# Kernel optimization log

Hardware: AMD Instinct MI355X
Metric: run time of the kernel (lower is better)

The kernel has to match this reference:

```python
import jax, jax.numpy as jnp
import numpy as np

TAU_MIN, TAU_MAX, TAU_SMALL, N_REF = 0.005, 0.1, 0.3, 4


def _l2norm(x, eps=1e-12):
    # matches torch F.normalize: x / max(||x||_2, eps)
    n = jnp.linalg.norm(x, axis=-1, keepdims=True)
    return x / jnp.maximum(n, eps)


def setup_inputs() -> dict:
    key = jax.random.key(0)
    k1, k2, k3 = jax.random.split(key, 3)
    B, C, H, W = 8, 384, 40, 40
    feats = jax.random.normal(k1, (B, C, H, W), dtype=jnp.float32)
    refs = jax.random.normal(k2, (N_REF, B, C, H, W), dtype=jnp.float32)
    sopm = jax.random.uniform(k3, (B, 1, 160, 160), dtype=jnp.float32)
    log_tau = jnp.array([np.log(0.03)], dtype=jnp.float32)
    alpha_raw = jnp.array([0.0], dtype=jnp.float32)
    return {"feats": feats, "refs": refs, "sopm": sopm,
            "log_tau": log_tau, "alpha_raw": alpha_raw}


def reference(feats, refs, sopm, log_tau, alpha_raw):
    B, C, H, W = feats.shape
    N = H * W
    # buffer contents and SOPM cache are detached in the torch module
    refs = jax.lax.stop_gradient(refs)
    sopm = jax.lax.stop_gradient(sopm)

    tau = jnp.clip(jnp.exp(log_tau[0]), TAU_MIN, TAU_MAX)
    alpha = jax.nn.sigmoid(alpha_raw[0])

    tokens = feats.reshape(B, C, N).transpose(0, 2, 1)   # [B, N, C]
    cur_n = _l2norm(tokens)

    n_ref = refs.shape[0]
    warped_sum = jnp.zeros_like(tokens)
    for r in range(n_ref):  # fixed small ref-frame loop (n_ref=4)
        ref_tok = refs[r].reshape(B, C, N).transpose(0, 2, 1)  # [B, N, C]
        ref_n = _l2norm(ref_tok)
        sim = jnp.einsum('bnc,bmc->bnm', cur_n, ref_n)          # cosine sims
        w = jax.nn.softmax(sim / tau, axis=-1)                  # [B, N, N]
        warped_sum = warped_sum + jnp.einsum('bnm,bmc->bnc', w, ref_tok)
    warped = warped_sum / n_ref

    # SOPM(t-1) -> bilinear resize (align_corners=False) -> threshold mask
    sopm_r = jax.image.resize(sopm, (B, 1, H, W), method='bilinear')
    mask = (sopm_r.reshape(B, 1, N).transpose(0, 2, 1) > TAU_SMALL).astype(feats.dtype)  # [B,N,1]

    alpha_eff = alpha  # full buffer: n_avail == n_ref
    fused = alpha_eff * warped + (1.0 - alpha_eff) * tokens
    enhanced = mask * fused + (1.0 - mask) * tokens
    return enhanced.transpose(0, 2, 1).reshape(B, C, H, W)
```

## Files before the change

### kernel.cpp

```cpp
#include <hip/hip_runtime.h>
#include <stdint.h>

#define B_  8
#define C_  384
#define N_  1600
#define R_  4
#define S_  160
#define HW_ 40

typedef float  f32x4  __attribute__((ext_vector_type(4)));
typedef __bf16 bf16x8 __attribute__((ext_vector_type(8)));
typedef long long i64t;

__device__ __forceinline__ unsigned short f2bf(float x){
  __bf16 h = (__bf16)x;
  return __builtin_bit_cast(unsigned short, h);
}
__device__ __forceinline__ float bf2f(unsigned short u){
  return __builtin_bit_cast(float, (uint32_t)u << 16);
}
__device__ __forceinline__ uint32_t pk_fp8x4(float a, float b, float c, float d){
  int lo = __builtin_amdgcn_cvt_pk_fp8_f32(a, b, 0, false);
  int hi = __builtin_amdgcn_cvt_pk_fp8_f32(c, d, 0, false);
  return (uint32_t)(lo & 0xffff) | ((uint32_t)hi << 16);
}

__device__ __forceinline__ void gload_lds16(const void* g, void* l){
  __builtin_amdgcn_global_load_lds(
      (const __attribute__((address_space(1))) uint32_t*)g,
      (__attribute__((address_space(3))) uint32_t*)l, 16, 0, 0);
}

__global__ void prep_kernel(const float* __restrict__ feats,
                            const float* __restrict__ refs,
                            unsigned char* __restrict__ Qb,
                            unsigned char* __restrict__ Kb,
                            unsigned short* __restrict__ Vb){
  int nt = blockIdx.x, mat = blockIdx.y;
  __shared__ unsigned short tile[64][386];
  __shared__ float ssp[64][17];
  __shared__ float inv_sh[64];
  int t = threadIdx.x;
  bool isref = (mat >= B_);
  const float* src = isref ? refs  + (size_t)(mat - B_) * C_ * N_
                           : feats + (size_t)mat * C_ * N_;
  int n4  = t & 15;
  int crb = t >> 4;
  float ss4[4] = {0.f, 0.f, 0.f, 0.f};
#pragma unroll
  for (int ct = 0; ct < 6; ++ct){
#pragma unroll
    for (int i = 0; i < 4; ++i){
      int c = ct * 64 + crb + 16 * i;
      size_t off = (size_t)c * N_ + nt * 64 + n4 * 4;
      float4 v = *(const float4*)(src + off);
      ushort4 o;
      o.x = f2bf(v.x); o.y = f2bf(v.y); o.z = f2bf(v.z); o.w = f2bf(v.w);
      if (isref){
        unsigned short* vdst = Vb + (size_t)(mat - B_) * C_ * N_;
        *(ushort4*)(vdst + off) = o;
      }
      tile[n4*4+0][c] = o.x;
      tile[n4*4+1][c] = o.y;
      tile[n4*4+2][c] = o.z;
      tile[n4*4+3][c] = o.w;
      ss4[0] += v.x * v.x;  ss4[1] += v.y * v.y;
      ss4[2] += v.z * v.z;  ss4[3] += v.w * v.w;
    }
  }
#pragma unroll
  for (int j = 0; j < 4; ++j) ssp[n4*4+j][crb] = ss4[j];
  __syncthreads();
  if (t < 64){
    float s = 0.f;
#pragma unroll
    for (int p = 0; p < 16; ++p) s += ssp[t][p];
    inv_sh[t] = 1.f / fmaxf(sqrtf(s), 1e-12f);
  }
  __syncthreads();
  unsigned char* dst = isref ? Kb + (size_t)(mat - B_) * N_ * C_
                             : Qb + (size_t)mat * N_ * C_;
#pragma unroll
  for (int i = 0; i < 4; ++i){
    int nr = (t >> 4) + 16 * i;
    float iv = inv_sh[nr];
    unsigned char* drow = dst + (size_t)(nt * 64 + nr) * C_;
#pragma unroll
    for (int ct = 0; ct < 6; ++ct){
      int c0 = ct * 64 + (t & 15) * 4;
      uint32_t a0 = *(const uint32_t*)(&tile[nr][c0]);
      uint32_t a1 = *(const uint32_t*)(&tile[nr][c0 + 2]);
      uint32_t pk = pk_fp8x4(bf2f((unsigned short)(a0 & 0xffff)) * iv,
                             bf2f((unsigned short)(a0 >> 16))    * iv,
                             bf2f((unsigned short)(a1 & 0xffff)) * iv,
                             bf2f((unsigned short)(a1 >> 16))    * iv);
      *(uint32_t*)(drow + c0) = pk;
    }
  }
}

__global__ void mask_kernel(const float* __restrict__ sopm,
                            float* __restrict__ maskp){
  int gid = blockIdx.x * 256 + threadIdx.x;
  int b = gid / N_, n = gid - b * N_;
  int oy = n / HW_, ox = n - oy * HW_;
  const float* sp = sopm + (size_t)b * S_ * S_;
  float cy = oy * 4 + 1.5f, cx = ox * 4 + 1.5f;
  int y0 = 4*oy - 2; if (y0 < 0) y0 = 0;
  int y1 = 4*oy + 5; if (y1 > S_-1) y1 = S_-1;
  int x0 = 4*ox - 2; if (x0 < 0) x0 = 0;
  int x1 = 4*ox + 5; if (x1 > S_-1) x1 = S_-1;
  float wsy = 0.f, wsx = 0.f;
  for (int j = y0; j <= y1; ++j) wsy += 1.f - fabsf(j - cy) * 0.25f;
  for (int j = x0; j <= x1; ++j) wsx += 1.f - fabsf(j - cx) * 0.25f;
  float acc = 0.f;
  for (int jy = y0; jy <= y1; ++jy){
    float wy = 1.f - fabsf(jy - cy) * 0.25f;
    float rs = 0.f;
    for (int jx = x0; jx <= x1; ++jx)
      rs += (1.f - fabsf(jx - cx) * 0.25f) * sp[jy * S_ + jx];
    acc += wy * rs;
  }
  float val = acc / (wsy * wsx);
  maskp[gid] = (val > 0.3f) ? 1.f : 0.f;
}

#define KB0_   0
#define KB1_   12288
#define VB_    24576
#define P_OFF  49152
#define LDS_SZ 53248

__global__ __launch_bounds__(256, 2) void attn_kernel(
    const unsigned char* __restrict__ Qb,
    const unsigned char* __restrict__ Kb,
    const unsigned short* __restrict__ Vb,
    const float* __restrict__ log_tau,
    unsigned short* __restrict__ Or)
{
  __shared__ __align__(16) char lds[LDS_SZ];
  int wg   = blockIdx.x;
  int orig = (wg & 7) * 100 + (wg >> 3);
  int qt   = orig % 25;
  int rb   = orig / 25;
  int b    = rb & 7;
  int tid  = threadIdx.x;
  int lane = tid & 63;
  int w    = tid >> 6;
  int mw   = w >> 1;
  int qw   = w & 1;
  int l15  = lane & 15;
  int lg   = lane >> 4;

  float tau = expf(log_tau[0]);
  tau = fminf(fmaxf(tau, 0.005f), 0.1f);
  float sc = 1.4426950408889634f / tau;

  i64t qreg[2][12];
#pragma unroll
  for (int qt2 = 0; qt2 < 2; ++qt2){
    const unsigned char* qp = Qb +
        ((size_t)b * N_ + qt * 64 + qw * 32 + qt2 * 16 + l15) * C_ + lg * 8;
#pragma unroll
    for (int ks = 0; ks < 12; ++ks)
      qreg[qt2][ks] = *(const i64t*)(qp + ks * 32);
  }

  f32x4 o[4][6];
#pragma unroll
  for (int i = 0; i < 4; ++i)
#pragma unroll
    for (int j = 0; j < 6; ++j) o[i][j] = (f32x4){0.f,0.f,0.f,0.f};
  float lsum0 = 0.f, lsum1 = 0.f;

  const unsigned char*  kmat = Kb + (size_t)rb * N_ * C_;
  const unsigned short* vmat = Vb + (size_t)rb * C_ * N_;
  char* Pb = lds + P_OFF;

  int koffB[3];
#pragma unroll
  for (int i = 0; i < 3; ++i){
    int L = (w * 3 + i) * 64 + lane;
    int m   = L / 24;
    int pos = L - m * 24;
    int cc  = (pos >> 3) * 8 + ((pos & 7) ^ (m & 7));
    koffB[i] = m * C_ + cc * 16;
  }
  int voff[6];
#pragma unroll
  for (int i = 0; i < 6; ++i){
    int chunk = (w * 6 + i) * 64 + lane;
    int line = chunk >> 3;
    int u    = (chunk & 7) ^ (line & 7);
    voff[i]  = (line * 2 + (u >> 2)) * N_ + (u & 3) * 8;
  }

  const int s_l  = (l15 >> 1) & 3;
  const int p_w0 = (qw*32      + l15) * 64 + (((2*mw + (lg >> 1)) ^ s_l) << 4) + (lg & 1) * 8;
  const int p_w1 = (qw*32 + 16 + l15) * 64 + (((2*mw + (lg >> 1)) ^ s_l) << 4) + (lg & 1) * 8;
  const int p_rc = ((lg ^ s_l) << 4) + l15 * 64;

  auto stageK = [&](int t, int buf){
    const unsigned char* kb = kmat + (size_t)t * 32 * C_;
    char* kdst = lds + (buf ? KB1_ : KB0_) + w * 3072;
#pragma unroll
    for (int i = 0; i < 3; ++i) gload_lds16(kb + koffB[i], kdst + i * 1024);
  };
  auto stageV = [&](int t){
    const unsigned short* vb = vmat + t * 32;
    char* vdst = lds + VB_ + w * 6144;
#pragma unroll
    for (int i = 0; i < 6; ++i) gload_lds16(vb + voff[i], vdst + i * 1024);
  };

  stageK(0, 0);
  stageV(0);
  stageK(1, 1);
  asm volatile("s_waitcnt vmcnt(9)" ::: "memory");
  __builtin_amdgcn_sched_barrier(0);
  __builtin_amdgcn_s_barrier();
  __builtin_amdgcn_sched_barrier(0);

  const int krow = (mw * 16 + l15);
  for (int mt = 0; mt < 50; ++mt){
    int cur = mt & 1;
    const char* kbR = lds + (cur ? KB1_ : KB0_);

    f32x4 s0 = {0.f,0.f,0.f,0.f}, s1 = {0.f,0.f,0.f,0.f};
    __builtin_amdgcn_s_setprio(1);
#pragma unroll
    for (int ks = 0; ks < 12; ++ks){
      int lc  = 2 * ks + (lg >> 1);
      int off = ((lc >> 3) * 8 + ((lc & 7) ^ (krow & 7))) * 16 + (lg & 1) * 8;
      i64t a = *(const i64t*)(kbR + krow * 384 + off);
      s0 = __builtin_amdgcn_mfma_f32_16x16x32_fp8_fp8(a, qreg[0][ks], s0, 0, 0, 0);
      s1 = __builtin_amdgcn_mfma_f32_16x16x32_fp8_fp8(a, qreg[1][ks], s1, 0, 0, 0);
    }
    __builtin_amdgcn_s_setprio(0);

    ushort4 pw0, pw1;
    {
      __bf16 h;
      float l0 = 0.f, l1 = 0.f;
      h = (__bf16)exp2f((s0[0]-1.f)*sc); l0 += (float)h; pw0.x = __builtin_bit_cast(unsigned short, h);
      h = (__bf16)exp2f((s0[1]-1.f)*sc); l0 += (float)h; pw0.y = __builtin_bit_cast(unsigned short, h);
      h = (__bf16)exp2f((s0[2]-1.f)*sc); l0 += (float)h; pw0.z = __builtin_bit_cast(unsigned short, h);
      h = (__bf16)exp2f((s0[3]-1.f)*sc); l0 += (float)h; pw0.w = __builtin_bit_cast(unsigned short, h);
      h = (__bf16)exp2f((s1[0]-1.f)*sc); l1 += (float)h; pw1.x = __builtin_bit_cast(unsigned short, h);
      h = (__bf16)exp2f((s1[1]-1.f)*sc); l1 += (float)h; pw1.y = __builtin_bit_cast(unsigned short, h);
      h = (__bf16)exp2f((s1[2]-1.f)*sc); l1 += (float)h; pw1.z = __builtin_bit_cast(unsigned short, h);
      h = (__bf16)exp2f((s1[3]-1.f)*sc); l1 += (float)h; pw1.w = __builtin_bit_cast(unsigned short, h);
      lsum0 += l0; lsum1 += l1;
    }
    *(ushort4*)(Pb + p_w0) = pw0;
    *(ushort4*)(Pb + p_w1) = pw1;
    asm volatile("s_waitcnt lgkmcnt(0) vmcnt(0)" ::: "memory");
    __builtin_amdgcn_sched_barrier(0);
    __builtin_amdgcn_s_barrier();
    __builtin_amdgcn_sched_barrier(0);

    int tk = (mt + 2 < 50) ? mt + 2 : mt;
    stageK(tk, cur);
    __builtin_amdgcn_sched_barrier(0);

    bf16x8 pa[4];
#pragma unroll
    for (int qf2 = 0; qf2 < 4; ++qf2)
      pa[qf2] = *(const bf16x8*)(Pb + qf2 * 1024 + p_rc);
    __builtin_amdgcn_s_setprio(1);
#pragma unroll
    for (int cf = 0; cf < 6; ++cf){
      int c  = w * 96 + cf * 16 + l15;
      int vo = (c >> 1) * 128 + (((lg | ((c & 1) << 2)) ^ ((c >> 1) & 7)) << 4);
      bf16x8 vf = *(const bf16x8*)(lds + VB_ + vo);
#pragma unroll
      for (int qf2 = 0; qf2 < 4; ++qf2)
        o[qf2][cf] = __builtin_amdgcn_mfma_f32_16x16x32_bf16(pa[qf2], vf, o[qf2][cf], 0, 0, 0);
    }
    __builtin_amdgcn_s_setprio(0);

    __builtin_amdgcn_sched_barrier(0);
    __builtin_amdgcn_s_barrier();
    __builtin_amdgcn_sched_barrier(0);

    int tv = (mt + 1 < 50) ? mt + 1 : 49;
    stageV(tv);
    __builtin_amdgcn_sched_barrier(0);
  }

  lsum0 += __shfl_xor(lsum0, 16, 64);
  lsum0 += __shfl_xor(lsum0, 32, 64);
  lsum1 += __shfl_xor(lsum1, 16, 64);
  lsum1 += __shfl_xor(lsum1, 32, 64);
  __syncthreads();
  float* lsh = (float*)lds;
  if (lg == 0){
    lsh[mw * 64 + qw * 32 + l15]      = lsum0;
    lsh[mw * 64 + qw * 32 + 16 + l15] = lsum1;
  }
  __syncthreads();
  float invl[4][4];
#pragma unroll
  for (int qf2 = 0; qf2 < 4; ++qf2)
#pragma unroll
    for (int rg = 0; rg < 4; ++rg){
      int q = qf2 * 16 + lg * 4 + rg;
      invl[qf2][rg] = 1.f / (lsh[q] + lsh[64 + q]);
    }

  int qbase = qt * 64;
  unsigned short* op = Or + ((size_t)rb * N_ + qbase) * C_ + w * 96 + l15;
#pragma unroll
  for (int qf2 = 0; qf2 < 4; ++qf2){
#pragma unroll
    for (int cf = 0; cf < 6; ++cf){
#pragma unroll
      for (int rg = 0; rg < 4; ++rg){
        int q = qf2 * 16 + lg * 4 + rg;
        op[(size_t)q * C_ + cf * 16] = f2bf(o[qf2][cf][rg] * invl[qf2][rg]);
      }
    }
  }
}

__global__ void combine_kernel(const unsigned short* __restrict__ Or,
                               const float* __restrict__ feats,
                               const float* __restrict__ maskp,
                               const float* __restrict__ alpha_raw,
                               float* __restrict__ out){
  int nt = blockIdx.x, ct = blockIdx.y, b = blockIdx.z;
  __shared__ float tile[64][65];
  float alpha = 1.f / (1.f + expf(-alpha_raw[0]));
  int t = threadIdx.x;
#pragma unroll
  for (int i = 0; i < 4; ++i){
    int chunk = t + 256 * i;
    int nr = chunk >> 4, c4 = chunk & 15;
    size_t base = ((size_t)b * N_ + nt * 64 + nr) * C_ + ct * 64 + c4 * 4;
    float4 s = {0.f,0.f,0.f,0.f};
#pragma unroll
    for (int r = 0; r < 4; ++r){
      ushort4 v = *(const ushort4*)(Or + (size_t)r * B_ * N_ * C_ + base);
      s.x += bf2f(v.x); s.y += bf2f(v.y); s.z += bf2f(v.z); s.w += bf2f(v.w);
    }
    tile[nr][c4*4+0] = s.x; tile[nr][c4*4+1] = s.y;
    tile[nr][c4*4+2] = s.z; tile[nr][c4*4+3] = s.w;
  }
  __syncthreads();
#pragma unroll
  for (int i = 0; i < 4; ++i){
    int chunk = t + 256 * i;
    int cr = chunk >> 4, n4 = chunk & 15;
    size_t fb = ((size_t)b * C_ + ct * 64 + cr) * N_ + nt * 64 + n4 * 4;
    float4 f  = *(const float4*)(feats + fb);
    float4 mk = *(const float4*)(maskp + (size_t)b * N_ + nt * 64 + n4 * 4);
    float4 ov;
    ov.x = f.x + mk.x * alpha * (tile[n4*4+0][cr] * 0.25f - f.x);
    ov.y = f.y + mk.y * alpha * (tile[n4*4+1][cr] * 0.25f - f.y);
    ov.z = f.z + mk.z * alpha * (tile[n4*4+2][cr] * 0.25f - f.z);
    ov.w = f.w + mk.w * alpha * (tile[n4*4+3][cr] * 0.25f - f.w);
    *(float4*)(out + fb) = ov;
  }
}

__global__ void poison_kernel(float* out, int n){
  int i = blockIdx.x * 256 + threadIdx.x;
  if (i < n) out[i] = 1.0e6f;
}

extern "C" void kernel_launch(void* const* d_in, const int* in_sizes, int n_in,
                              void* d_out, int out_size, void* d_ws, size_t ws_size,
                              hipStream_t stream){
  const float* feats     = (const float*)d_in[0];
  const float* refs      = (const float*)d_in[1];
  const float* sopm      = (const float*)d_in[2];
  const float* log_tau   = (const float*)d_in[3];
  const float* alpha_raw = (const float*)d_in[4];
  float* out = (float*)d_out;

  const size_t SZ_MASK = (size_t)B_ * N_ * 4;
  const size_t SZ_QB   = (size_t)B_ * N_ * C_;
  const size_t SZ_KB   = (size_t)R_ * B_ * N_ * C_;
  const size_t SZ_VB   = (size_t)R_ * B_ * N_ * C_ * 2;
  const size_t SZ_OR   = (size_t)R_ * B_ * N_ * C_ * 2;
  const size_t need = SZ_MASK + SZ_QB + SZ_KB + SZ_VB + SZ_OR;

  if (ws_size < need){
    poison_kernel<<<(out_size + 255) / 256, 256, 0, stream>>>(out, out_size);
    return;
  }
  char* ws = (char*)d_ws;
  float*          maskp = (float*)ws;
  unsigned char*  Qb    = (unsigned char*)(ws + SZ_MASK);
  unsigned char*  Kb    = (unsigned char*)(ws + SZ_MASK + SZ_QB);
  unsigned short* Vb    = (unsigned short*)(ws + SZ_MASK + SZ_QB + SZ_KB);
  unsigned short* Or    = (unsigned short*)(ws + SZ_MASK + SZ_QB + SZ_KB + SZ_VB);

  mask_kernel   <<<50, 256, 0, stream>>>(sopm, maskp);
  prep_kernel   <<<dim3(25, 40), 256, 0, stream>>>(feats, refs, Qb, Kb, Vb);
  attn_kernel   <<<800, 256, 0, stream>>>(Qb, Kb, Vb, log_tau, Or);
  combine_kernel<<<dim3(25, 6, 8), 256, 0, stream>>>(Or, feats, maskp, alpha_raw, out);
}
```

Before: 202.3 us.

## Split attention work across 8 waves per block with smaller per-wave tiles

Moves the attention kernel from 256 to 512 threads per block. Each wave now owns 16 queries instead of 32 for the QK step and 48 channels instead of 96 for the PV step, which halves the per-wave accumulator and Q registers. The goal is more resident waves per CU to hide latency. In exchange, K staging is limited to four waves and the prologue prefetch becomes a full wait, which reduces overlap, while the per-block barriers now synchronise more waves.

```diff
diff --git a/kernel.cpp b/kernel.cpp
--- a/kernel.cpp
+++ b/kernel.cpp
@@ -131,7 +131,7 @@
 #define P_OFF  49152
 #define LDS_SZ 53248
 
-__global__ __launch_bounds__(256, 2) void attn_kernel(
+__global__ __launch_bounds__(512, 4) void attn_kernel(
     const unsigned char* __restrict__ Qb,
     const unsigned char* __restrict__ Kb,
     const unsigned short* __restrict__ Vb,
@@ -147,8 +147,8 @@
   int tid  = threadIdx.x;
   int lane = tid & 63;
   int w    = tid >> 6;
-  int mw   = w >> 1;
-  int qw   = w & 1;
+  int mw   = w >> 2;
+  int qw   = w & 3;
   int l15  = lane & 15;
   int lg   = lane >> 4;
 
@@ -156,22 +156,21 @@
   tau = fminf(fmaxf(tau, 0.005f), 0.1f);
   float sc = 1.4426950408889634f / tau;
 
-  i64t qreg[2][12];
-#pragma unroll
-  for (int qt2 = 0; qt2 < 2; ++qt2){
+  i64t qreg[12];
+  {
     const unsigned char* qp = Qb +
-        ((size_t)b * N_ + qt * 64 + qw * 32 + qt2 * 16 + l15) * C_ + lg * 8;
+        ((size_t)b * N_ + qt * 64 + qw * 16 + l15) * C_ + lg * 8;
 #pragma unroll
     for (int ks = 0; ks < 12; ++ks)
-      qreg[qt2][ks] = *(const i64t*)(qp + ks * 32);
-  }
-
-  f32x4 o[4][6];
+      qreg[ks] = *(const i64t*)(qp + ks * 32);
+  }
+
+  f32x4 o[4][3];
 #pragma unroll
   for (int i = 0; i < 4; ++i)
 #pragma unroll
-    for (int j = 0; j < 6; ++j) o[i][j] = (f32x4){0.f,0.f,0.f,0.f};
-  float lsum0 = 0.f, lsum1 = 0.f;
+    for (int j = 0; j < 3; ++j) o[i][j] = (f32x4){0.f,0.f,0.f,0.f};
+  float lsum = 0.f;
 
   const unsigned char*  kmat = Kb + (size_t)rb * N_ * C_;
   const unsigned short* vmat = Vb + (size_t)rb * C_ * N_;
@@ -180,80 +179,75 @@
   int koffB[3];
 #pragma unroll
   for (int i = 0; i < 3; ++i){
-    int L = (w * 3 + i) * 64 + lane;
+    int L = ((w & 3) * 3 + i) * 64 + lane;
     int m   = L / 24;
     int pos = L - m * 24;
     int cc  = (pos >> 3) * 8 + ((pos & 7) ^ (m & 7));
     koffB[i] = m * C_ + cc * 16;
   }
-  int voff[6];
-#pragma unroll
-  for (int i = 0; i < 6; ++i){
-    int chunk = (w * 6 + i) * 64 + lane;
+  int voff[3];
+#pragma unroll
+  for (int i = 0; i < 3; ++i){
+    int chunk = (w * 3 + i) * 64 + lane;
     int line = chunk >> 3;
     int u    = (chunk & 7) ^ (line & 7);
     voff[i]  = (line * 2 + (u >> 2)) * N_ + (u & 3) * 8;
   }
 
   const int s_l  = (l15 >> 1) & 3;
-  const int p_w0 = (qw*32      + l15) * 64 + (((2*mw + (lg >> 1)) ^ s_l) << 4) + (lg & 1) * 8;
-  const int p_w1 = (qw*32 + 16 + l15) * 64 + (((2*mw + (lg >> 1)) ^ s_l) << 4) + (lg & 1) * 8;
+  const int p_w  = (qw*16 + l15) * 64 + (((mw*2 + (lg >> 1)) ^ s_l) << 4) + (lg & 1) * 8;
   const int p_rc = ((lg ^ s_l) << 4) + l15 * 64;
 
   auto stageK = [&](int t, int buf){
-    const unsigned char* kb = kmat + (size_t)t * 32 * C_;
-    char* kdst = lds + (buf ? KB1_ : KB0_) + w * 3072;
-#pragma unroll
-    for (int i = 0; i < 3; ++i) gload_lds16(kb + koffB[i], kdst + i * 1024);
+    if (w < 4){
+      const unsigned char* kb = kmat + (size_t)t * 32 * C_;
+      char* kdst = lds + (buf ? KB1_ : KB0_) + w * 3072;
+#pragma unroll
+      for (int i = 0; i < 3; ++i) gload_lds16(kb + koffB[i], kdst + i * 1024);
+    }
   };
   auto stageV = [&](int t){
     const unsigned short* vb = vmat + t * 32;
-    char* vdst = lds + VB_ + w * 6144;
-#pragma unroll
-    for (int i = 0; i < 6; ++i) gload_lds16(vb + voff[i], vdst + i * 1024);
+    char* vdst = lds + VB_ + w * 3072;
+#pragma unroll
+    for (int i = 0; i < 3; ++i) gload_lds16(vb + voff[i], vdst + i * 1024);
   };
 
   stageK(0, 0);
   stageV(0);
-  stageK(1, 1);
-  asm volatile("s_waitcnt vmcnt(9)" ::: "memory");
+  asm volatile("s_waitcnt vmcnt(0)" ::: "memory");
   __builtin_amdgcn_sched_barrier(0);
   __builtin_amdgcn_s_barrier();
   __builtin_amdgcn_sched_barrier(0);
+  stageK(1, 1);
 
   const int krow = (mw * 16 + l15);
   for (int mt = 0; mt < 50; ++mt){
     int cur = mt & 1;
     const char* kbR = lds + (cur ? KB1_ : KB0_);
 
-    f32x4 s0 = {0.f,0.f,0.f,0.f}, s1 = {0.f,0.f,0.f,0.f};
+    f32x4 s0 = {0.f,0.f,0.f,0.f};
     __builtin_amdgcn_s_setprio(1);
 #pragma unroll
     for (int ks = 0; ks < 12; ++ks){
       int lc  = 2 * ks + (lg >> 1);
       int off = ((lc >> 3) * 8 + ((lc & 7) ^ (krow & 7))) * 16 + (lg & 1) * 8;
       i64t a = *(const i64t*)(kbR + krow * 384 + off);
-      s0 = __builtin_amdgcn_mfma_f32_16x16x32_fp8_fp8(a, qreg[0][ks], s0, 0, 0, 0);
-      s1 = __builtin_amdgcn_mfma_f32_16x16x32_fp8_fp8(a, qreg[1][ks], s1, 0, 0, 0);
+      s0 = __builtin_amdgcn_mfma_f32_16x16x32_fp8_fp8(a, qreg[ks], s0, 0, 0, 0);
     }
     __builtin_amdgcn_s_setprio(0);
 
-    ushort4 pw0, pw1;
+    ushort4 pw;
     {
       __bf16 h;
-      float l0 = 0.f, l1 = 0.f;
-      h = (__bf16)exp2f((s0[0]-1.f)*sc); l0 += (float)h; pw0.x = __builtin_bit_cast(unsigned short, h);
-      h = (__bf16)exp2f((s0[1]-1.f)*sc); l0 += (float)h; pw0.y = __builtin_bit_cast(unsigned short, h);
-      h = (__bf16)exp2f((s0[2]-1.f)*sc); l0 += (float)h; pw0.z = __builtin_bit_cast(unsigned short, h);
-      h = (__bf16)exp2f((s0[3]-1.f)*sc); l0 += (float)h; pw0.w = __builtin_bit_cast(unsigned short, h);
-      h = (__bf16)exp2f((s1[0]-1.f)*sc); l1 += (float)h; pw1.x = __builtin_bit_cast(unsigned short, h);
-      h = (__bf16)exp2f((s1[1]-1.f)*sc); l1 += (float)h; pw1.y = __builtin_bit_cast(unsigned short, h);
-      h = (__bf16)exp2f((s1[2]-1.f)*sc); l1 += (float)h; pw1.z = __builtin_bit_cast(unsigned short, h);
-      h = (__bf16)exp2f((s1[3]-1.f)*sc); l1 += (float)h; pw1.w = __builtin_bit_cast(unsigned short, h);
-      lsum0 += l0; lsum1 += l1;
-    }
-    *(ushort4*)(Pb + p_w0) = pw0;
-    *(ushort4*)(Pb + p_w1) = pw1;
+      float l0 = 0.f;
+      h = (__bf16)exp2f((s0[0]-1.f)*sc); l0 += (float)h; pw.x = __builtin_bit_cast(unsigned short, h);
+      h = (__bf16)exp2f((s0[1]-1.f)*sc); l0 += (float)h; pw.y = __builtin_bit_cast(unsigned short, h);
+      h = (__bf16)exp2f((s0[2]-1.f)*sc); l0 += (float)h; pw.z = __builtin_bit_cast(unsigned short, h);
+      h = (__bf16)exp2f((s0[3]-1.f)*sc); l0 += (float)h; pw.w = __builtin_bit_cast(unsigned short, h);
+      lsum += l0;
+    }
+    *(ushort4*)(Pb + p_w) = pw;
     asm volatile("s_waitcnt lgkmcnt(0) vmcnt(0)" ::: "memory");
     __builtin_amdgcn_sched_barrier(0);
     __builtin_amdgcn_s_barrier();
@@ -269,8 +263,8 @@
       pa[qf2] = *(const bf16x8*)(Pb + qf2 * 1024 + p_rc);
     __builtin_amdgcn_s_setprio(1);
 #pragma unroll
-    for (int cf = 0; cf < 6; ++cf){
-      int c  = w * 96 + cf * 16 + l15;
+    for (int cf = 0; cf < 3; ++cf){
+      int c  = w * 48 + cf * 16 + l15;
       int vo = (c >> 1) * 128 + (((lg | ((c & 1) << 2)) ^ ((c >> 1) & 7)) << 4);
       bf16x8 vf = *(const bf16x8*)(lds + VB_ + vo);
 #pragma unroll
@@ -288,16 +282,11 @@
     __builtin_amdgcn_sched_barrier(0);
   }
 
-  lsum0 += __shfl_xor(lsum0, 16, 64);
-  lsum0 += __shfl_xor(lsum0, 32, 64);
-  lsum1 += __shfl_xor(lsum1, 16, 64);
-  lsum1 += __shfl_xor(lsum1, 32, 64);
+  lsum += __shfl_xor(lsum, 16, 64);
+  lsum += __shfl_xor(lsum, 32, 64);
   __syncthreads();
   float* lsh = (float*)lds;
-  if (lg == 0){
-    lsh[mw * 64 + qw * 32 + l15]      = lsum0;
-    lsh[mw * 64 + qw * 32 + 16 + l15] = lsum1;
-  }
+  if (lg == 0) lsh[mw * 64 + qw * 16 + l15] = lsum;
   __syncthreads();
   float invl[4][4];
 #pragma unroll
@@ -309,11 +298,11 @@
     }
 
   int qbase = qt * 64;
-  unsigned short* op = Or + ((size_t)rb * N_ + qbase) * C_ + w * 96 + l15;
+  unsigned short* op = Or + ((size_t)rb * N_ + qbase) * C_ + w * 48 + l15;
 #pragma unroll
   for (int qf2 = 0; qf2 < 4; ++qf2){
 #pragma unroll
-    for (int cf = 0; cf < 6; ++cf){
+    for (int cf = 0; cf < 3; ++cf){
 #pragma unroll
       for (int rg = 0; rg < 4; ++rg){
         int q = qf2 * 16 + lg * 4 + rg;
@@ -398,6 +387,6 @@
 
   mask_kernel   <<<50, 256, 0, stream>>>(sopm, maskp);
   prep_kernel   <<<dim3(25, 40), 256, 0, stream>>>(feats, refs, Qb, Kb, Vb);
-  attn_kernel   <<<800, 256, 0, stream>>>(Qb, Kb, Vb, log_tau, Or);
+  attn_kernel   <<<800, 512, 0, stream>>>(Qb, Kb, Vb, log_tau, Or);
   combine_kernel<<<dim3(25, 6, 8), 256, 0, stream>>>(Or, feats, maskp, alpha_raw, out);
 }
```

Measured after the change: 217.6 us. +7.5%, slower.

## Double the KV tile to 64 keys per iteration and single-buffer K

Applied to the files above, without the earlier changes.

The attention loop now handles 64 key positions per iteration instead of 32, cutting the iteration count and barrier count in half. Each wave computes two 16-row key fragments for the QK product and two k-slices for the PV product. K goes from double buffering to a single larger buffer, and V and P layouts are reswizzled for the 64-wide tiles. This raises LDS use to 80KB, which may limit occupancy at two blocks per CU, and it adds a barrier after the V stage, which reduces overlap between loads and compute.

```diff
diff --git a/kernel.cpp b/kernel.cpp
--- a/kernel.cpp
+++ b/kernel.cpp
@@ -125,11 +125,10 @@
   maskp[gid] = (val > 0.3f) ? 1.f : 0.f;
 }
 
-#define KB0_   0
-#define KB1_   12288
+#define KB_    0
 #define VB_    24576
-#define P_OFF  49152
-#define LDS_SZ 53248
+#define P_OFF  73728
+#define LDS_SZ 81920
 
 __global__ __launch_bounds__(256, 2) void attn_kernel(
     const unsigned char* __restrict__ Qb,
@@ -151,6 +150,7 @@
   int qw   = w & 1;
   int l15  = lane & 15;
   int lg   = lane >> 4;
+  const int s7 = l15 & 7;
 
   float tau = expf(log_tau[0]);
   tau = fminf(fmaxf(tau, 0.005f), 0.1f);
@@ -177,105 +177,124 @@
   const unsigned short* vmat = Vb + (size_t)rb * C_ * N_;
   char* Pb = lds + P_OFF;
 
-  int koffB[3];
-#pragma unroll
-  for (int i = 0; i < 3; ++i){
-    int L = (w * 3 + i) * 64 + lane;
+  int koffB[6];
+#pragma unroll
+  for (int i = 0; i < 6; ++i){
+    int L = (w * 6 + i) * 64 + lane;
     int m   = L / 24;
     int pos = L - m * 24;
     int cc  = (pos >> 3) * 8 + ((pos & 7) ^ (m & 7));
     koffB[i] = m * C_ + cc * 16;
   }
-  int voff[6];
-#pragma unroll
-  for (int i = 0; i < 6; ++i){
-    int chunk = (w * 6 + i) * 64 + lane;
-    int line = chunk >> 3;
-    int u    = (chunk & 7) ^ (line & 7);
-    voff[i]  = (line * 2 + (u >> 2)) * N_ + (u & 3) * 8;
-  }
-
-  const int s_l  = (l15 >> 1) & 3;
-  const int p_w0 = (qw*32      + l15) * 64 + (((2*mw + (lg >> 1)) ^ s_l) << 4) + (lg & 1) * 8;
-  const int p_w1 = (qw*32 + 16 + l15) * 64 + (((2*mw + (lg >> 1)) ^ s_l) << 4) + (lg & 1) * 8;
-  const int p_rc = ((lg ^ s_l) << 4) + l15 * 64;
-
-  auto stageK = [&](int t, int buf){
-    const unsigned char* kb = kmat + (size_t)t * 32 * C_;
-    char* kdst = lds + (buf ? KB1_ : KB0_) + w * 3072;
-#pragma unroll
-    for (int i = 0; i < 3; ++i) gload_lds16(kb + koffB[i], kdst + i * 1024);
+  int voff[12];
+#pragma unroll
+  for (int i = 0; i < 12; ++i){
+    int chunk = (w * 12 + i) * 64 + lane;
+    int c = chunk >> 3;
+    int u = (chunk & 7) ^ (c & 7);
+    voff[i] = c * N_ + u * 8;
+  }
+
+  int p_wo[2][2];
+#pragma unroll
+  for (int mi = 0; mi < 2; ++mi)
+#pragma unroll
+    for (int qi = 0; qi < 2; ++qi)
+      p_wo[mi][qi] = (qw*32 + qi*16 + l15) * 128 +
+                     (((mw*4 + mi*2 + (lg >> 1)) ^ s7) << 4) + (lg & 1) * 8;
+
+  auto stageK = [&](int t){
+    const unsigned char* kb = kmat + (size_t)t * 64 * C_;
+#pragma unroll
+    for (int i = 0; i < 6; ++i)
+      gload_lds16(kb + koffB[i], lds + KB_ + (w * 6 + i) * 1024);
   };
   auto stageV = [&](int t){
-    const unsigned short* vb = vmat + t * 32;
-    char* vdst = lds + VB_ + w * 6144;
-#pragma unroll
-    for (int i = 0; i < 6; ++i) gload_lds16(vb + voff[i], vdst + i * 1024);
+    const unsigned short* vb = vmat + t * 64;
+#pragma unroll
+    for (int i = 0; i < 12; ++i)
+      gload_lds16(vb + voff[i], lds + VB_ + (w * 12 + i) * 1024);
   };
 
-  stageK(0, 0);
+  stageK(0);
   stageV(0);
-  stageK(1, 1);
-  asm volatile("s_waitcnt vmcnt(9)" ::: "memory");
+  asm volatile("s_waitcnt vmcnt(0)" ::: "memory");
   __builtin_amdgcn_sched_barrier(0);
   __builtin_amdgcn_s_barrier();
   __builtin_amdgcn_sched_barrier(0);
 
-  const int krow = (mw * 16 + l15);
-  for (int mt = 0; mt < 50; ++mt){
-    int cur = mt & 1;
-    const char* kbR = lds + (cur ? KB1_ : KB0_);
-
-    f32x4 s0 = {0.f,0.f,0.f,0.f}, s1 = {0.f,0.f,0.f,0.f};
+  const int krow0 = (mw * 32 + l15) * 384;
+  const int krow1 = (mw * 32 + 16 + l15) * 384;
+  for (int mt = 0; mt < 25; ++mt){
+    f32x4 s00 = {0.f,0.f,0.f,0.f}, s01 = {0.f,0.f,0.f,0.f};
+    f32x4 s10 = {0.f,0.f,0.f,0.f}, s11 = {0.f,0.f,0.f,0.f};
     __builtin_amdgcn_s_setprio(1);
 #pragma unroll
     for (int ks = 0; ks < 12; ++ks){
       int lc  = 2 * ks + (lg >> 1);
-      int off = ((lc >> 3) * 8 + ((lc & 7) ^ (krow & 7))) * 16 + (lg & 1) * 8;
-      i64t a = *(const i64t*)(kbR + krow * 384 + off);
-      s0 = __builtin_amdgcn_mfma_f32_16x16x32_fp8_fp8(a, qreg[0][ks], s0, 0, 0, 0);
-      s1 = __builtin_amdgcn_mfma_f32_16x16x32_fp8_fp8(a, qreg[1][ks], s1, 0, 0, 0);
+      int off = ((lc >> 3) * 8 + ((lc & 7) ^ s7)) * 16 + (lg & 1) * 8;
+      i64t a0 = *(const i64t*)(lds + KB_ + krow0 + off);
+      i64t a1 = *(const i64t*)(lds + KB_ + krow1 + off);
+      s00 = __builtin_amdgcn_mfma_f32_16x16x32_fp8_fp8(a0, qreg[0][ks], s00, 0, 0, 0);
+      s01 = __builtin_amdgcn_mfma_f32_16x16x32_fp8_fp8(a0, qreg[1][ks], s01, 0, 0, 0);
+      s10 = __builtin_amdgcn_mfma_f32_16x16x32_fp8_fp8(a1, qreg[0][ks], s10, 0, 0, 0);
+      s11 = __builtin_amdgcn_mfma_f32_16x16x32_fp8_fp8(a1, qreg[1][ks], s11, 0, 0, 0);
     }
     __builtin_amdgcn_s_setprio(0);
 
-    ushort4 pw0, pw1;
     {
       __bf16 h;
       float l0 = 0.f, l1 = 0.f;
-      h = (__bf16)exp2f((s0[0]-1.f)*sc); l0 += (float)h; pw0.x = __builtin_bit_cast(unsigned short, h);
-      h = (__bf16)exp2f((s0[1]-1.f)*sc); l0 += (float)h; pw0.y = __builtin_bit_cast(unsigned short, h);
-      h = (__bf16)exp2f((s0[2]-1.f)*sc); l0 += (float)h; pw0.z = __builtin_bit_cast(unsigned short, h);
-      h = (__bf16)exp2f((s0[3]-1.f)*sc); l0 += (float)h; pw0.w = __builtin_bit_cast(unsigned short, h);
-      h = (__bf16)exp2f((s1[0]-1.f)*sc); l1 += (float)h; pw1.x = __builtin_bit_cast(unsigned short, h);
-      h = (__bf16)exp2f((s1[1]-1.f)*sc); l1 += (float)h; pw1.y = __builtin_bit_cast(unsigned short, h);
-      h = (__bf16)exp2f((s1[2]-1.f)*sc); l1 += (float)h; pw1.z = __builtin_bit_cast(unsigned short, h);
-      h = (__bf16)exp2f((s1[3]-1.f)*sc); l1 += (float)h; pw1.w = __builtin_bit_cast(unsigned short, h);
+      ushort4 pw;
+      h = (__bf16)exp2f((s00[0]-1.f)*sc); l0 += (float)h; pw.x = __builtin_bit_cast(unsigned short, h);
+      h = (__bf16)exp2f((s00[1]-1.f)*sc); l0 += (float)h; pw.y = __builtin_bit_cast(unsigned short, h);
+      h = (__bf16)exp2f((s00[2]-1.f)*sc); l0 += (float)h; pw.z = __builtin_bit_cast(unsigned short, h);
+      h = (__bf16)exp2f((s00[3]-1.f)*sc); l0 += (float)h; pw.w = __builtin_bit_cast(unsigned short, h);
+      *(ushort4*)(Pb + p_wo[0][0]) = pw;
+      h = (__bf16)exp2f((s01[0]-1.f)*sc); l1 += (float)h; pw.x = __builtin_bit_cast(unsigned short, h);
+      h = (__bf16)exp2f((s01[1]-1.f)*sc); l1 += (float)h; pw.y = __builtin_bit_cast(unsigned short, h);
+      h = (__bf16)exp2f((s01[2]-1.f)*sc); l1 += (float)h; pw.z = __builtin_bit_cast(unsigned short, h);
+      h = (__bf16)exp2f((s01[3]-1.f)*sc); l1 += (float)h; pw.w = __builtin_bit_cast(unsigned short, h);
+      *(ushort4*)(Pb + p_wo[0][1]) = pw;
+      h = (__bf16)exp2f((s10[0]-1.f)*sc); l0 += (float)h; pw.x = __builtin_bit_cast(unsigned short, h);
+      h = (__bf16)exp2f((s10[1]-1.f)*sc); l0 += (float)h; pw.y = __builtin_bit_cast(unsigned short, h);
+      h = (__bf16)exp2f((s10[2]-1.f)*sc); l0 += (float)h; pw.z = __builtin_bit_cast(unsigned short, h);
+      h = (__bf16)exp2f((s10[3]-1.f)*sc); l0 += (float)h; pw.w = __builtin_bit_cast(unsigned short, h);
+      *(ushort4*)(Pb + p_wo[1][0]) = pw;
+      h = (__bf16)exp2f((s11[0]-1.f)*sc); l1 += (float)h; pw.x = __builtin_bit_cast(unsigned short, h);
+      h = (__bf16)exp2f((s11[1]-1.f)*sc); l1 += (float)h; pw.y = __builtin_bit_cast(unsigned short, h);
+      h = (__bf16)exp2f((s11[2]-1.f)*sc); l1 += (float)h; pw.z = __builtin_bit_cast(unsigned short, h);
+      h = (__bf16)exp2f((s11[3]-1.f)*sc); l1 += (float)h; pw.w = __builtin_bit_cast(unsigned short, h);
+      *(ushort4*)(Pb + p_wo[1][1]) = pw;
       lsum0 += l0; lsum1 += l1;
     }
-    *(ushort4*)(Pb + p_w0) = pw0;
-    *(ushort4*)(Pb + p_w1) = pw1;
     asm volatile("s_waitcnt lgkmcnt(0) vmcnt(0)" ::: "memory");
     __builtin_amdgcn_sched_barrier(0);
     __builtin_amdgcn_s_barrier();
     __builtin_amdgcn_sched_barrier(0);
 
-    int tk = (mt + 2 < 50) ? mt + 2 : mt;
-    stageK(tk, cur);
-    __builtin_amdgcn_sched_barrier(0);
-
-    bf16x8 pa[4];
+    int tk = (mt + 1 < 25) ? mt + 1 : mt;
+    stageK(tk);
+    __builtin_amdgcn_sched_barrier(0);
+
+    bf16x8 pa[4][2];
 #pragma unroll
     for (int qf2 = 0; qf2 < 4; ++qf2)
-      pa[qf2] = *(const bf16x8*)(Pb + qf2 * 1024 + p_rc);
+#pragma unroll
+      for (int s = 0; s < 2; ++s)
+        pa[qf2][s] = *(const bf16x8*)(Pb + (qf2*16 + l15) * 128 +
+                                      (((s*4 + lg) ^ s7) << 4));
     __builtin_amdgcn_s_setprio(1);
 #pragma unroll
     for (int cf = 0; cf < 6; ++cf){
-      int c  = w * 96 + cf * 16 + l15;
-      int vo = (c >> 1) * 128 + (((lg | ((c & 1) << 2)) ^ ((c >> 1) & 7)) << 4);
-      bf16x8 vf = *(const bf16x8*)(lds + VB_ + vo);
-#pragma unroll
-      for (int qf2 = 0; qf2 < 4; ++qf2)
-        o[qf2][cf] = __builtin_amdgcn_mfma_f32_16x16x32_bf16(pa[qf2], vf, o[qf2][cf], 0, 0, 0);
+      int vbase = VB_ + (w*96 + cf*16 + l15) * 128;
+#pragma unroll
+      for (int s = 0; s < 2; ++s){
+        bf16x8 vf = *(const bf16x8*)(lds + vbase + (((s*4 + lg) ^ s7) << 4));
+#pragma unroll
+        for (int qf2 = 0; qf2 < 4; ++qf2)
+          o[qf2][cf] = __builtin_amdgcn_mfma_f32_16x16x32_bf16(pa[qf2][s], vf, o[qf2][cf], 0, 0, 0);
+      }
     }
     __builtin_amdgcn_s_setprio(0);
 
@@ -283,8 +302,11 @@
     __builtin_amdgcn_s_barrier();
     __builtin_amdgcn_sched_barrier(0);
 
-    int tv = (mt + 1 < 50) ? mt + 1 : 49;
+    int tv = (mt + 1 < 25) ? mt + 1 : mt;
     stageV(tv);
+    asm volatile("s_waitcnt vmcnt(12)" ::: "memory");
+    __builtin_amdgcn_sched_barrier(0);
+    __builtin_amdgcn_s_barrier();
     __builtin_amdgcn_sched_barrier(0);
   }
 
```

Measured after the change: 215.2 us. 6.4% more time.
